# Optimization experiments

Hardware: AMD Instinct MI355X
Metric: run time of the kernel (lower is better)

The kernel has to match this reference:

```python
import jax, jax.numpy as jnp
import numpy as np

B, T, C = 4, 2048, 1024
H = 16
D = C // H  # head_dim = 64


def setup_inputs() -> dict:
    key = jax.random.key(0)
    ks = jax.random.split(key, 9)
    s = 1.0 / np.sqrt(C)
    return {
        "x": jax.random.normal(ks[0], (B, T, C), dtype=jnp.float32),
        "Wk": jax.random.uniform(ks[1], (C, C), jnp.float32, -s, s),
        "bk": jax.random.uniform(ks[2], (C,), jnp.float32, -s, s),
        "Wq": jax.random.uniform(ks[3], (C, C), jnp.float32, -s, s),
        "bq": jax.random.uniform(ks[4], (C,), jnp.float32, -s, s),
        "Wv": jax.random.uniform(ks[5], (C, C), jnp.float32, -s, s),
        "bv": jax.random.uniform(ks[6], (C,), jnp.float32, -s, s),
        "Wp": jax.random.uniform(ks[7], (C, C), jnp.float32, -s, s),
        "bp": jax.random.uniform(ks[8], (C,), jnp.float32, -s, s),
    }


def reference(x, Wk, bk, Wq, bq, Wv, bv, Wp, bp):
    # projections -> (B, H, T, D)
    def split_heads(y):
        return y.reshape(B, T, H, D).transpose(0, 2, 1, 3)

    k = split_heads(x @ Wk.T + bk)
    q = split_heads(x @ Wq.T + bq)
    v = split_heads(x @ Wv.T + bv)

    att = jnp.einsum("bhtd,bhsd->bhts", q, k) / np.sqrt(D).astype(np.float32)
    causal = jnp.tril(jnp.ones((T, T), dtype=bool))
    att = jnp.where(causal, att, -jnp.inf)
    att = jax.nn.softmax(att, axis=-1)

    y = jnp.einsum("bhts,bhsd->bhtd", att, v)  # (B,H,T,D)
    y = y.transpose(0, 2, 1, 3).reshape(B, T, C)
    return y @ Wp.T + bp
```

## Files before the change

kernel.cpp:

```cpp
#include <hip/hip_runtime.h>
#include <hip/hip_bf16.h>

typedef unsigned short u16;
typedef unsigned int u32;
typedef short short8 __attribute__((ext_vector_type(8)));
typedef short short4v __attribute__((ext_vector_type(4)));
typedef float f32x4 __attribute__((ext_vector_type(4)));

#define MFMA16(a, b, c) __builtin_amdgcn_mfma_f32_16x16x32_bf16((a), (b), (c), 0, 0, 0)

constexpr int kB = 4, kT = 2048, kC = 1024, kH = 16, kD = 64;
constexpr int kBT = kB * kT;
constexpr long kQKV = (long)kB * kH * kT * kD;
constexpr float kSC = 0.125f * 1.4426950408889634f;

__device__ inline u16 f2bf(float f) {
    __hip_bfloat16 h = __float2bfloat16(f);
    return *reinterpret_cast<u16*>(&h);
}
__device__ inline u32 pkbf_trunc(float lo, float hi) {
    return __builtin_amdgcn_perm(__builtin_bit_cast(u32, hi),
                                 __builtin_bit_cast(u32, lo), 0x07060302u);
}
__device__ inline u32 pkbf_rne(float lo, float hi) {
    return ((u32)f2bf(hi) << 16) | (u32)f2bf(lo);
}

__device__ inline void cp16(const u16* g, u16* l) {
    __builtin_amdgcn_global_load_lds(
        (const __attribute__((address_space(1))) unsigned int*)g,
        (__attribute__((address_space(3))) unsigned int*)l, 16, 0, 0);
}

__global__ __launch_bounds__(256) void cast_kernel(
    const float* __restrict__ x,  const float* __restrict__ Wk,
    const float* __restrict__ Wq, const float* __restrict__ Wv,
    const float* __restrict__ Wp,
    u16* __restrict__ xb, u16* __restrict__ wkb, u16* __restrict__ wqb,
    u16* __restrict__ wvb, u16* __restrict__ wpb)
{
    const long id = (long)blockIdx.x * 256 + threadIdx.x;
    const float* src;
    u16* dst;
    long off;
    if (id < 2097152) {
        src = x; dst = xb; off = id;
    } else {
        const long w = (id - 2097152) >> 18;
        off = (id - 2097152) & 262143;
        src = (w == 0) ? Wk : (w == 1) ? Wq : (w == 2) ? Wv : Wp;
        dst = (w == 0) ? wkb : (w == 1) ? wqb : (w == 2) ? wvb : wpb;
    }
    f32x4 v = *(const f32x4*)&src[off * 4];
    short4v s = {(short)f2bf(v[0]), (short)f2bf(v[1]),
                 (short)f2bf(v[2]), (short)f2bf(v[3])};
    *(short4v*)&dst[off * 4] = s;
}

__global__ __launch_bounds__(256) void qkv_gemm_bf16(
    const u16* __restrict__ xb,
    const u16* __restrict__ wkb, const u16* __restrict__ wqb,
    const u16* __restrict__ wvb,
    const float* __restrict__ bk, const float* __restrict__ bq,
    const float* __restrict__ bv,
    u16* __restrict__ kw, u16* __restrict__ qw, u16* __restrict__ vw)
{
    __shared__ u16 As[128 * 32];
    __shared__ u16 Bs[128 * 32];
    const int tid = threadIdx.x;
    const int lane = tid & 63;
    const int wid = tid >> 6;
    const int l15 = lane & 15;
    const int quad = lane >> 4;
    const int m0 = blockIdx.x * 128;
    const int n0 = blockIdx.y * 128;
    const int z = blockIdx.z;

    const u16* W = (z == 0) ? wkb : (z == 1) ? wqb : wvb;
    const float* bias = (z == 0) ? bk : (z == 1) ? bq : bv;

    f32x4 zero = {0.f, 0.f, 0.f, 0.f};
    f32x4 acc[4][4];
#pragma unroll
    for (int i = 0; i < 4; ++i)
#pragma unroll
        for (int j = 0; j < 4; ++j) acc[i][j] = zero;

    const int wm = (wid & 1) * 64;
    const int wn = (wid >> 1) * 64;

    const int sRow = tid >> 2;
    const int sCol = (tid & 3) * 8;
    const int ldsOff = sRow * 32 + sCol;

    for (int k0 = 0; k0 < kC; k0 += 32) {
        cp16(&xb[(long)(m0 + sRow) * kC + k0 + sCol],      &As[ldsOff]);
        cp16(&xb[(long)(m0 + 64 + sRow) * kC + k0 + sCol], &As[64 * 32 + ldsOff]);
        cp16(&W[(long)(n0 + sRow) * kC + k0 + sCol],       &Bs[ldsOff]);
        cp16(&W[(long)(n0 + 64 + sRow) * kC + k0 + sCol],  &Bs[64 * 32 + ldsOff]);
        __syncthreads();
        short8 af[4], bfr[4];
#pragma unroll
        for (int mt = 0; mt < 4; ++mt)
            af[mt] = *(const short8*)&As[(wm + mt * 16 + l15) * 32 + quad * 8];
#pragma unroll
        for (int nt = 0; nt < 4; ++nt)
            bfr[nt] = *(const short8*)&Bs[(wn + nt * 16 + l15) * 32 + quad * 8];
#pragma unroll
        for (int mt = 0; mt < 4; ++mt)
#pragma unroll
            for (int nt = 0; nt < 4; ++nt)
                acc[mt][nt] = MFMA16(af[mt], bfr[nt], acc[mt][nt]);
        __syncthreads();
    }

    const float scale = (z == 1) ? kSC : 1.0f;
#pragma unroll
    for (int nt = 0; nt < 4; ++nt) {
        const int n = n0 + wn + nt * 16 + l15;
        const float bias_f = bias[n];
        const int h = n >> 6, d = n & 63;
#pragma unroll
        for (int mt = 0; mt < 4; ++mt) {
#pragma unroll
            for (int r = 0; r < 4; ++r) {
                const int m = m0 + wm + mt * 16 + quad * 4 + r;
                const int b = m >> 11, t = m & 2047;
                const float v = (acc[mt][nt][r] + bias_f) * scale;
                const int bh = b * kH + h;
                if (z == 2) {
                    vw[((long)bh * kD + d) * kT + t] = f2bf(v);
                } else {
                    u16* dst = (z == 0) ? kw : qw;
                    dst[((long)bh * kT + t) * kD + d] = f2bf(v);
                }
            }
        }
    }
}

__global__ __launch_bounds__(256) void qkv_gemm_kernel(
    const float* __restrict__ x,
    const float* __restrict__ Wk, const float* __restrict__ bk,
    const float* __restrict__ Wq, const float* __restrict__ bq,
    const float* __restrict__ Wv, const float* __restrict__ bv,
    u16* __restrict__ kw, u16* __restrict__ qw, u16* __restrict__ vw)
{
    __shared__ u16 As[128 * 32];
    __shared__ u16 Bs[128 * 32];
    const int tid = threadIdx.x;
    const int lane = tid & 63;
    const int wid = tid >> 6;
    const int l15 = lane & 15;
    const int quad = lane >> 4;
    const int m0 = blockIdx.x * 128;
    const int n0 = blockIdx.y * 128;
    const int z = blockIdx.z;

    const float* W = (z == 0) ? Wk : (z == 1) ? Wq : Wv;
    const float* bias = (z == 0) ? bk : (z == 1) ? bq : bv;

    f32x4 zero = {0.f, 0.f, 0.f, 0.f};
    f32x4 acc[4][4];
#pragma unroll
    for (int i = 0; i < 4; ++i)
#pragma unroll
        for (int j = 0; j < 4; ++j) acc[i][j] = zero;

    const int wm = (wid & 1) * 64;
    const int wn = (wid >> 1) * 64;
    const int row4 = tid >> 3;
    const int col4 = (tid & 7) * 4;

    for (int k0 = 0; k0 < kC; k0 += 32) {
#pragma unroll
        for (int p = 0; p < 4; ++p) {
            const int r = p * 32 + row4;
            f32x4 xa = *(const f32x4*)&x[(long)(m0 + r) * kC + k0 + col4];
            f32x4 wa = *(const f32x4*)&W[(long)(n0 + r) * kC + k0 + col4];
            short4v xs = {(short)f2bf(xa[0]), (short)f2bf(xa[1]),
                          (short)f2bf(xa[2]), (short)f2bf(xa[3])};
            short4v wsv = {(short)f2bf(wa[0]), (short)f2bf(wa[1]),
                           (short)f2bf(wa[2]), (short)f2bf(wa[3])};
            *(short4v*)&As[r * 32 + col4] = xs;
            *(short4v*)&Bs[r * 32 + col4] = wsv;
        }
        __syncthreads();
        short8 af[4], bfr[4];
#pragma unroll
        for (int mt = 0; mt < 4; ++mt)
            af[mt] = *(const short8*)&As[(wm + mt * 16 + l15) * 32 + quad * 8];
#pragma unroll
        for (int nt = 0; nt < 4; ++nt)
            bfr[nt] = *(const short8*)&Bs[(wn + nt * 16 + l15) * 32 + quad * 8];
#pragma unroll
        for (int mt = 0; mt < 4; ++mt)
#pragma unroll
            for (int nt = 0; nt < 4; ++nt)
                acc[mt][nt] = MFMA16(af[mt], bfr[nt], acc[mt][nt]);
        __syncthreads();
    }

    const float scale = (z == 1) ? kSC : 1.0f;
#pragma unroll
    for (int nt = 0; nt < 4; ++nt) {
        const int n = n0 + wn + nt * 16 + l15;
        const float bias_f = bias[n];
        const int h = n >> 6, d = n & 63;
#pragma unroll
        for (int mt = 0; mt < 4; ++mt) {
#pragma unroll
            for (int r = 0; r < 4; ++r) {
                const int m = m0 + wm + mt * 16 + quad * 4 + r;
                const int b = m >> 11, t = m & 2047;
                const float v = (acc[mt][nt][r] + bias_f) * scale;
                const int bh = b * kH + h;
                if (z == 2) {
                    vw[((long)bh * kD + d) * kT + t] = f2bf(v);
                } else {
                    u16* dst = (z == 0) ? kw : qw;
                    dst[((long)bh * kT + t) * kD + d] = f2bf(v);
                }
            }
        }
    }
}

__global__ __launch_bounds__(256) void attn_kernel(
    const u16* qw, const u16* kw, const u16* vw, u16* ow)
{
    __shared__ u16 Ks[2][64 * 64];
    __shared__ u16 VT[2][64 * 64];
    __shared__ u16 Pb[64 * 64];

    const int tid = threadIdx.x;
    const int lane = tid & 63;
    const int wid = tid >> 6;
    const int l15 = lane & 15;
    const int quad = lane >> 4;
    const int id = blockIdx.x;
    const int bh = id & 63;
    const int pr = id >> 6;

    const float NEG = -1.0e30f;
    f32x4 zero = {0.f, 0.f, 0.f, 0.f};
    const short8 onesf = {(short)0x3F80, (short)0x3F80, (short)0x3F80, (short)0x3F80,
                          (short)0x3F80, (short)0x3F80, (short)0x3F80, (short)0x3F80};

    const int r0 = tid >> 3;
    const int cc = tid & 7;
    const int r1 = r0 + 32;
    const int sw0 = r0 * 64 + ((cc ^ (r0 & 7)) * 8);
    const int sw1 = r1 * 64 + ((cc ^ (r1 & 7)) * 8);
    const int c0e = cc * 8;

    const int rl7 = l15 & 7;

    const u16* kbase = kw + (long)bh * kT * kD;
    const u16* vbase = vw + (long)bh * kD * kT;

#pragma unroll
    for (int ph = 0; ph < 2; ++ph) {
        const int qt64 = ph ? (31 - pr) : pr;
        const int tw = qt64 * 64 + wid * 16;

        short8 qf0, qf1;
        {
            const u16* qp = qw + ((long)bh * kT + tw + l15) * kD;
            qf0 = *(const short8*)&qp[quad * 8];
            qf1 = *(const short8*)&qp[32 + quad * 8];
        }

        f32x4 oacc[4];
#pragma unroll
        for (int mo = 0; mo < 4; ++mo) oacc[mo] = zero;
        f32x4 lsum = zero;

        const int n_st = qt64 + 1;

        const u16* kp0 = kbase + (long)r0 * kD + c0e;
        const u16* kp1 = kbase + (long)r1 * kD + c0e;
        const u16* vp0 = vbase + (long)r0 * kT + c0e;
        const u16* vp1 = vbase + (long)r1 * kT + c0e;
        short8 ka = *(const short8*)kp0;
        short8 kb = *(const short8*)kp1;
        short8 va = *(const short8*)vp0;
        short8 vb = *(const short8*)vp1;
        kp0 += 64 * kD; kp1 += 64 * kD;
        vp0 += 64;      vp1 += 64;
        __syncthreads();
        *(short8*)&Ks[0][sw0] = ka;
        *(short8*)&Ks[0][sw1] = kb;
        *(short8*)&VT[0][sw0] = va;
        *(short8*)&VT[0][sw1] = vb;
        if (n_st > 1) {
            ka = *(const short8*)kp0;
            kb = *(const short8*)kp1;
            va = *(const short8*)vp0;
            vb = *(const short8*)vp1;
            kp0 += 64 * kD; kp1 += 64 * kD;
            vp0 += 64;      vp1 += 64;
        }

        for (int st = 0; st < n_st; ++st) {
            __syncthreads();
            const int cur = st & 1;
            if (st + 1 < n_st) {
                const int nxt = cur ^ 1;
                *(short8*)&Ks[nxt][sw0] = ka;
                *(short8*)&Ks[nxt][sw1] = kb;
                *(short8*)&VT[nxt][sw0] = va;
                *(short8*)&VT[nxt][sw1] = vb;
            }
            if (st + 2 < n_st) {
                ka = *(const short8*)kp0;
                kb = *(const short8*)kp1;
                va = *(const short8*)vp0;
                vb = *(const short8*)vp1;
                kp0 += 64 * kD; kp1 += 64 * kD;
                vp0 += 64;      vp1 += 64;
            }

            short8 kf[4][2];
#pragma unroll
            for (int ms = 0; ms < 4; ++ms) {
                const int row = ms * 16 + l15;
#pragma unroll
                for (int k2 = 0; k2 < 2; ++k2)
                    kf[ms][k2] = *(const short8*)
                        &Ks[cur][row * 64 + (((k2 * 4 + quad) ^ rl7) * 8)];
            }
            f32x4 sacc[4];
#pragma unroll
            for (int ms = 0; ms < 4; ++ms) {
                sacc[ms] = MFMA16(kf[ms][0], qf0, zero);
                sacc[ms] = MFMA16(kf[ms][1], qf1, sacc[ms]);
            }

            if (st == n_st - 1) {
                const int tl = wid * 16 + l15;
#pragma unroll
                for (int ms = 0; ms < 4; ++ms)
#pragma unroll
                    for (int r = 0; r < 4; ++r)
                        if (ms * 16 + quad * 4 + r > tl) sacc[ms][r] = NEG;
            }

            const int prow = wid * 16 + l15;
#pragma unroll
            for (int ms = 0; ms < 4; ++ms) {
                const float p0 = exp2f(sacc[ms][0]);
                const float p1 = exp2f(sacc[ms][1]);
                const float p2 = exp2f(sacc[ms][2]);
                const float p3 = exp2f(sacc[ms][3]);
                uint2 pk;
                pk.x = pkbf_trunc(p0, p1);
                pk.y = pkbf_trunc(p2, p3);
                const int chunk = (ms * 2 + (quad >> 1)) ^ rl7;
                *(uint2*)&Pb[prow * 64 + chunk * 8 + (quad & 1) * 4] = pk;
            }

            short8 pf0 = *(const short8*)&Pb[prow * 64 + ((quad ^ rl7) * 8)];
            short8 pf1 = *(const short8*)&Pb[prow * 64 + (((4 + quad) ^ rl7) * 8)];
            lsum = MFMA16(onesf, pf0, lsum);
            lsum = MFMA16(onesf, pf1, lsum);
#pragma unroll
            for (int mo = 0; mo < 4; ++mo) {
                const int row = mo * 16 + l15;
                short8 vf0 = *(const short8*)
                    &VT[cur][row * 64 + ((quad ^ rl7) * 8)];
                short8 vf1 = *(const short8*)
                    &VT[cur][row * 64 + (((4 + quad) ^ rl7) * 8)];
                oacc[mo] = MFMA16(vf0, pf0, oacc[mo]);
                oacc[mo] = MFMA16(vf1, pf1, oacc[mo]);
            }
        }

        const float inv = 1.0f / lsum[0];
        const int t = tw + l15;
        u16* op = ow + ((long)bh * kT + t) * kD;
#pragma unroll
        for (int mo = 0; mo < 4; ++mo) {
            uint2 ov;
            ov.x = pkbf_rne(oacc[mo][0] * inv, oacc[mo][1] * inv);
            ov.y = pkbf_rne(oacc[mo][2] * inv, oacc[mo][3] * inv);
            *(uint2*)&op[mo * 16 + quad * 4] = ov;
        }
    }
}

__global__ __launch_bounds__(256) void out_gemm_bf16(
    const u16* __restrict__ ob, const u16* __restrict__ wpb,
    const float* __restrict__ bp, float* __restrict__ out)
{
    __shared__ u16 As[128 * 32];
    __shared__ u16 Bs[128 * 32];
    const int tid = threadIdx.x;
    const int lane = tid & 63;
    const int wid = tid >> 6;
    const int l15 = lane & 15;
    const int quad = lane >> 4;
    const int m0 = blockIdx.x * 128;
    const int n0 = blockIdx.y * 128;

    f32x4 zero = {0.f, 0.f, 0.f, 0.f};
    f32x4 acc[4][4];
#pragma unroll
    for (int i = 0; i < 4; ++i)
#pragma unroll
        for (int j = 0; j < 4; ++j) acc[i][j] = zero;

    const int wm = (wid & 1) * 64;
    const int wn = (wid >> 1) * 64;

    const int sRow = tid >> 2;
    const int sCol = (tid & 3) * 8;
    const int ldsOff = sRow * 32 + sCol;

    for (int k0 = 0; k0 < kC; k0 += 32) {
        const int h = k0 >> 6;
        const int d = (k0 & 63) + sCol;
        {
            const int m = m0 + sRow, b = m >> 11, t = m & 2047;
            cp16(&ob[(((long)b * kH + h) * kT + t) * kD + d], &As[ldsOff]);
        }
        {
            const int m = m0 + 64 + sRow, b = m >> 11, t = m & 2047;
            cp16(&ob[(((long)b * kH + h) * kT + t) * kD + d], &As[64 * 32 + ldsOff]);
        }
        cp16(&wpb[(long)(n0 + sRow) * kC + k0 + sCol],      &Bs[ldsOff]);
        cp16(&wpb[(long)(n0 + 64 + sRow) * kC + k0 + sCol], &Bs[64 * 32 + ldsOff]);
        __syncthreads();
        short8 af[4], bfr[4];
#pragma unroll
        for (int mt = 0; mt < 4; ++mt)
            af[mt] = *(const short8*)&As[(wm + mt * 16 + l15) * 32 + quad * 8];
#pragma unroll
        for (int nt = 0; nt < 4; ++nt)
            bfr[nt] = *(const short8*)&Bs[(wn + nt * 16 + l15) * 32 + quad * 8];
#pragma unroll
        for (int mt = 0; mt < 4; ++mt)
#pragma unroll
            for (int nt = 0; nt < 4; ++nt)
                acc[mt][nt] = MFMA16(af[mt], bfr[nt], acc[mt][nt]);
        __syncthreads();
    }

#pragma unroll
    for (int nt = 0; nt < 4; ++nt) {
        const int n = n0 + wn + nt * 16 + l15;
        const float bias_f = bp[n];
#pragma unroll
        for (int mt = 0; mt < 4; ++mt) {
#pragma unroll
            for (int r = 0; r < 4; ++r) {
                const int m = m0 + wm + mt * 16 + quad * 4 + r;
                out[(long)m * kC + n] = acc[mt][nt][r] + bias_f;
            }
        }
    }
}

__global__ __launch_bounds__(256) void out_gemm_kernel(
    const u16* __restrict__ ow, const float* __restrict__ Wp,
    const float* __restrict__ bp, float* __restrict__ out)
{
    __shared__ u16 As[128 * 32];
    __shared__ u16 Bs[128 * 32];
    const int tid = threadIdx.x;
    const int lane = tid & 63;
    const int wid = tid >> 6;
    const int l15 = lane & 15;
    const int quad = lane >> 4;
    const int m0 = blockIdx.x * 128;
    const int n0 = blockIdx.y * 128;

    f32x4 zero = {0.f, 0.f, 0.f, 0.f};
    f32x4 acc[4][4];
#pragma unroll
    for (int i = 0; i < 4; ++i)
#pragma unroll
        for (int j = 0; j < 4; ++j) acc[i][j] = zero;

    const int wm = (wid & 1) * 64;
    const int wn = (wid >> 1) * 64;

    const int r0 = tid >> 2;
    const int kkA = (tid & 3) * 8;
    const int r1 = r0 + 64;
    const int row4 = tid >> 3;
    const int col4 = (tid & 7) * 4;

    for (int k0 = 0; k0 < kC; k0 += 32) {
        {
            const int m = m0 + r0, b = m >> 11, t = m & 2047;
            const int kk = k0 + kkA, h = kk >> 6, d = kk & 63;
            *(short8*)&As[r0 * 32 + kkA] =
                *(const short8*)&ow[(((long)b * kH + h) * kT + t) * kD + d];
        }
        {
            const int m = m0 + r1, b = m >> 11, t = m & 2047;
            const int kk = k0 + kkA, h = kk >> 6, d = kk & 63;
            *(short8*)&As[r1 * 32 + kkA] =
                *(const short8*)&ow[(((long)b * kH + h) * kT + t) * kD + d];
        }
#pragma unroll
        for (int p = 0; p < 4; ++p) {
            const int r = p * 32 + row4;
            f32x4 wa = *(const f32x4*)&Wp[(long)(n0 + r) * kC + k0 + col4];
            short4v wsv = {(short)f2bf(wa[0]), (short)f2bf(wa[1]),
                           (short)f2bf(wa[2]), (short)f2bf(wa[3])};
            *(short4v*)&Bs[r * 32 + col4] = wsv;
        }
        __syncthreads();
        short8 af[4], bfr[4];
#pragma unroll
        for (int mt = 0; mt < 4; ++mt)
            af[mt] = *(const short8*)&As[(wm + mt * 16 + l15) * 32 + quad * 8];
#pragma unroll
        for (int nt = 0; nt < 4; ++nt)
            bfr[nt] = *(const short8*)&Bs[(wn + nt * 16 + l15) * 32 + quad * 8];
#pragma unroll
        for (int mt = 0; mt < 4; ++mt)
#pragma unroll
            for (int nt = 0; nt < 4; ++nt)
                acc[mt][nt] = MFMA16(af[mt], bfr[nt], acc[mt][nt]);
        __syncthreads();
    }

#pragma unroll
    for (int nt = 0; nt < 4; ++nt) {
        const int n = n0 + wn + nt * 16 + l15;
        const float bias_f = bp[n];
#pragma unroll
        for (int mt = 0; mt < 4; ++mt) {
#pragma unroll
            for (int r = 0; r < 4; ++r) {
                const int m = m0 + wm + mt * 16 + quad * 4 + r;
                out[(long)m * kC + n] = acc[mt][nt][r] + bias_f;
            }
        }
    }
}

extern "C" void kernel_launch(void* const* d_in, const int* in_sizes, int n_in,
                              void* d_out, int out_size, void* d_ws, size_t ws_size,
                              hipStream_t stream) {
    const float* x  = (const float*)d_in[0];
    const float* Wk = (const float*)d_in[1];
    const float* bk = (const float*)d_in[2];
    const float* Wq = (const float*)d_in[3];
    const float* bq = (const float*)d_in[4];
    const float* Wv = (const float*)d_in[5];
    const float* bv = (const float*)d_in[6];
    const float* Wp = (const float*)d_in[7];
    const float* bp = (const float*)d_in[8];
    float* out = (float*)d_out;

    u16* ws = (u16*)d_ws;
    const size_t kNeed = 72ull * 1024 * 1024;

    if (ws_size >= kNeed) {
        u16* k_ws = ws;
        u16* q_ws = ws + kQKV;
        u16* v_ws = ws + 2 * kQKV;
        u16* xb   = ws + 3 * kQKV;
        u16* o_ws = xb;
        u16* wkb  = ws + 4 * kQKV;
        u16* wqb  = wkb + (long)kC * kC;
        u16* wvb  = wqb + (long)kC * kC;
        u16* wpb  = wvb + (long)kC * kC;

        cast_kernel<<<12288, 256, 0, stream>>>(x, Wk, Wq, Wv, Wp,
                                               xb, wkb, wqb, wvb, wpb);
        qkv_gemm_bf16<<<dim3(kBT / 128, kC / 128, 3), 256, 0, stream>>>(
            xb, wkb, wqb, wvb, bk, bq, bv, k_ws, q_ws, v_ws);
        attn_kernel<<<1024, 256, 0, stream>>>(q_ws, k_ws, v_ws, o_ws);
        out_gemm_bf16<<<dim3(kBT / 128, kC / 128), 256, 0, stream>>>(
            o_ws, wpb, bp, out);
    } else {
        u16* k_ws = ws;
        u16* q_ws = ws + kQKV;
        u16* v_ws = ws + 2 * kQKV;
        u16* o_ws = q_ws;

        qkv_gemm_kernel<<<dim3(kBT / 128, kC / 128, 3), 256, 0, stream>>>(
            x, Wk, bk, Wq, bq, Wv, bv, k_ws, q_ws, v_ws);
        attn_kernel<<<1024, 256, 0, stream>>>(q_ws, k_ws, v_ws, o_ws);
        out_gemm_kernel<<<dim3(kBT / 128, kC / 128), 256, 0, stream>>>(
            o_ws, Wp, bp, out);
    }
}
```

Baseline: 282.7 us.

## Halve attention block to two waves each handling 32 query rows with async K/V staging

The attention kernel now runs with 128 threads, and each wave processes two 16-row query groups. Each K and V fragment read from shared memory is therefore reused across two MFMA groups, which halves LDS fragment traffic per unit of work. K/V tile loads switch from register-staged global loads to a cp16 helper writing directly into the swizzled LDS buffers. s_setprio hints are placed around the MFMA sections. The trade-off is higher register pressure per wave and fewer waves per block to hide latency, and the change relies on a cp16 helper defined elsewhere.

```diff
diff --git a/kernel.cpp b/kernel.cpp
--- a/kernel.cpp
+++ b/kernel.cpp
@@ -226,7 +226,7 @@
     }
 }
 
-__global__ __launch_bounds__(256) void attn_kernel(
+__global__ __launch_bounds__(128, 2) void attn_kernel(
     const u16* qw, const u16* kw, const u16* vw, u16* ow)
 {
     __shared__ u16 Ks[2][64 * 64];
@@ -247,144 +247,146 @@
     const short8 onesf = {(short)0x3F80, (short)0x3F80, (short)0x3F80, (short)0x3F80,
                           (short)0x3F80, (short)0x3F80, (short)0x3F80, (short)0x3F80};
 
-    const int r0 = tid >> 3;
-    const int cc = tid & 7;
-    const int r1 = r0 + 32;
-    const int sw0 = r0 * 64 + ((cc ^ (r0 & 7)) * 8);
-    const int sw1 = r1 * 64 + ((cc ^ (r1 & 7)) * 8);
-    const int c0e = cc * 8;
-
     const int rl7 = l15 & 7;
 
     const u16* kbase = kw + (long)bh * kT * kD;
     const u16* vbase = vw + (long)bh * kD * kT;
 
+    const u16* kp[4];
+    const u16* vp[4];
+#pragma unroll
+    for (int q = 0; q < 4; ++q) {
+        const int slot = q * 128 + tid;
+        const int row = slot >> 3;
+        const int c = slot & 7;
+        const int off = (c ^ (row & 7)) * 8;
+        kp[q] = kbase + (long)row * kD + off;
+        vp[q] = vbase + (long)row * kT + off;
+    }
+
+    auto stage = [&](int buf, int st) {
+        u16* kd = Ks[buf];
+        u16* vd = VT[buf];
+#pragma unroll
+        for (int q = 0; q < 4; ++q) {
+            cp16(kp[q] + (long)st * (64 * kD), kd + (q * 128 + tid) * 8);
+            cp16(vp[q] + st * 64,              vd + (q * 128 + tid) * 8);
+        }
+    };
+
 #pragma unroll
     for (int ph = 0; ph < 2; ++ph) {
         const int qt64 = ph ? (31 - pr) : pr;
-        const int tw = qt64 * 64 + wid * 16;
-
-        short8 qf0, qf1;
-        {
-            const u16* qp = qw + ((long)bh * kT + tw + l15) * kD;
-            qf0 = *(const short8*)&qp[quad * 8];
-            qf1 = *(const short8*)&qp[32 + quad * 8];
-        }
-
-        f32x4 oacc[4];
-#pragma unroll
-        for (int mo = 0; mo < 4; ++mo) oacc[mo] = zero;
-        f32x4 lsum = zero;
-
+        const int tw = qt64 * 64 + wid * 32;
         const int n_st = qt64 + 1;
 
-        const u16* kp0 = kbase + (long)r0 * kD + c0e;
-        const u16* kp1 = kbase + (long)r1 * kD + c0e;
-        const u16* vp0 = vbase + (long)r0 * kT + c0e;
-        const u16* vp1 = vbase + (long)r1 * kT + c0e;
-        short8 ka = *(const short8*)kp0;
-        short8 kb = *(const short8*)kp1;
-        short8 va = *(const short8*)vp0;
-        short8 vb = *(const short8*)vp1;
-        kp0 += 64 * kD; kp1 += 64 * kD;
-        vp0 += 64;      vp1 += 64;
-        __syncthreads();
-        *(short8*)&Ks[0][sw0] = ka;
-        *(short8*)&Ks[0][sw1] = kb;
-        *(short8*)&VT[0][sw0] = va;
-        *(short8*)&VT[0][sw1] = vb;
-        if (n_st > 1) {
-            ka = *(const short8*)kp0;
-            kb = *(const short8*)kp1;
-            va = *(const short8*)vp0;
-            vb = *(const short8*)vp1;
-            kp0 += 64 * kD; kp1 += 64 * kD;
-            vp0 += 64;      vp1 += 64;
-        }
+        __syncthreads();
+        stage(0, 0);
+
+        short8 qf[2][2];
+#pragma unroll
+        for (int g = 0; g < 2; ++g) {
+            const u16* qp = qw + ((long)bh * kT + tw + g * 16 + l15) * kD;
+            qf[g][0] = *(const short8*)&qp[quad * 8];
+            qf[g][1] = *(const short8*)&qp[32 + quad * 8];
+        }
+
+        f32x4 oacc[4][2];
+#pragma unroll
+        for (int mo = 0; mo < 4; ++mo)
+#pragma unroll
+            for (int g = 0; g < 2; ++g) oacc[mo][g] = zero;
+        f32x4 lsum[2] = {zero, zero};
 
         for (int st = 0; st < n_st; ++st) {
             __syncthreads();
             const int cur = st & 1;
-            if (st + 1 < n_st) {
-                const int nxt = cur ^ 1;
-                *(short8*)&Ks[nxt][sw0] = ka;
-                *(short8*)&Ks[nxt][sw1] = kb;
-                *(short8*)&VT[nxt][sw0] = va;
-                *(short8*)&VT[nxt][sw1] = vb;
-            }
-            if (st + 2 < n_st) {
-                ka = *(const short8*)kp0;
-                kb = *(const short8*)kp1;
-                va = *(const short8*)vp0;
-                vb = *(const short8*)vp1;
-                kp0 += 64 * kD; kp1 += 64 * kD;
-                vp0 += 64;      vp1 += 64;
-            }
-
-            short8 kf[4][2];
+            if (st + 1 < n_st) stage(cur ^ 1, st + 1);
+
+            const u16* K_ = Ks[cur];
+            const u16* V_ = VT[cur];
+
+            f32x4 sacc[4][2];
+            __builtin_amdgcn_s_setprio(1);
 #pragma unroll
             for (int ms = 0; ms < 4; ++ms) {
                 const int row = ms * 16 + l15;
-#pragma unroll
-                for (int k2 = 0; k2 < 2; ++k2)
-                    kf[ms][k2] = *(const short8*)
-                        &Ks[cur][row * 64 + (((k2 * 4 + quad) ^ rl7) * 8)];
-            }
-            f32x4 sacc[4];
-#pragma unroll
-            for (int ms = 0; ms < 4; ++ms) {
-                sacc[ms] = MFMA16(kf[ms][0], qf0, zero);
-                sacc[ms] = MFMA16(kf[ms][1], qf1, sacc[ms]);
-            }
+                short8 kf0 = *(const short8*)&K_[row * 64 + ((quad ^ rl7) * 8)];
+                short8 kf1 = *(const short8*)&K_[row * 64 + (((4 + quad) ^ rl7) * 8)];
+#pragma unroll
+                for (int g = 0; g < 2; ++g) {
+                    sacc[ms][g] = MFMA16(kf0, qf[g][0], zero);
+                    sacc[ms][g] = MFMA16(kf1, qf[g][1], sacc[ms][g]);
+                }
+            }
+            __builtin_amdgcn_s_setprio(0);
 
             if (st == n_st - 1) {
-                const int tl = wid * 16 + l15;
-#pragma unroll
-                for (int ms = 0; ms < 4; ++ms)
-#pragma unroll
-                    for (int r = 0; r < 4; ++r)
-                        if (ms * 16 + quad * 4 + r > tl) sacc[ms][r] = NEG;
-            }
-
-            const int prow = wid * 16 + l15;
-#pragma unroll
-            for (int ms = 0; ms < 4; ++ms) {
-                const float p0 = exp2f(sacc[ms][0]);
-                const float p1 = exp2f(sacc[ms][1]);
-                const float p2 = exp2f(sacc[ms][2]);
-                const float p3 = exp2f(sacc[ms][3]);
-                uint2 pk;
-                pk.x = pkbf_trunc(p0, p1);
-                pk.y = pkbf_trunc(p2, p3);
-                const int chunk = (ms * 2 + (quad >> 1)) ^ rl7;
-                *(uint2*)&Pb[prow * 64 + chunk * 8 + (quad & 1) * 4] = pk;
-            }
-
-            short8 pf0 = *(const short8*)&Pb[prow * 64 + ((quad ^ rl7) * 8)];
-            short8 pf1 = *(const short8*)&Pb[prow * 64 + (((4 + quad) ^ rl7) * 8)];
-            lsum = MFMA16(onesf, pf0, lsum);
-            lsum = MFMA16(onesf, pf1, lsum);
+#pragma unroll
+                for (int g = 0; g < 2; ++g) {
+                    const int tl = wid * 32 + g * 16 + l15;
+#pragma unroll
+                    for (int ms = 0; ms < 4; ++ms)
+#pragma unroll
+                        for (int r = 0; r < 4; ++r)
+                            if (ms * 16 + quad * 4 + r > tl) sacc[ms][g][r] = NEG;
+                }
+            }
+
+#pragma unroll
+            for (int g = 0; g < 2; ++g) {
+                const int prow = wid * 32 + g * 16 + l15;
+#pragma unroll
+                for (int ms = 0; ms < 4; ++ms) {
+                    const float p0 = exp2f(sacc[ms][g][0]);
+                    const float p1 = exp2f(sacc[ms][g][1]);
+                    const float p2 = exp2f(sacc[ms][g][2]);
+                    const float p3 = exp2f(sacc[ms][g][3]);
+                    uint2 pk;
+                    pk.x = pkbf_trunc(p0, p1);
+                    pk.y = pkbf_trunc(p2, p3);
+                    const int chunk = (ms * 2 + (quad >> 1)) ^ rl7;
+                    *(uint2*)&Pb[prow * 64 + chunk * 8 + (quad & 1) * 4] = pk;
+                }
+            }
+
+            short8 pf[2][2];
+#pragma unroll
+            for (int g = 0; g < 2; ++g) {
+                const int prow = wid * 32 + g * 16 + l15;
+                pf[g][0] = *(const short8*)&Pb[prow * 64 + ((quad ^ rl7) * 8)];
+                pf[g][1] = *(const short8*)&Pb[prow * 64 + (((4 + quad) ^ rl7) * 8)];
+                lsum[g] = MFMA16(onesf, pf[g][0], lsum[g]);
+                lsum[g] = MFMA16(onesf, pf[g][1], lsum[g]);
+            }
+
+            __builtin_amdgcn_s_setprio(1);
 #pragma unroll
             for (int mo = 0; mo < 4; ++mo) {
                 const int row = mo * 16 + l15;
-                short8 vf0 = *(const short8*)
-                    &VT[cur][row * 64 + ((quad ^ rl7) * 8)];
-                short8 vf1 = *(const short8*)
-                    &VT[cur][row * 64 + (((4 + quad) ^ rl7) * 8)];
-                oacc[mo] = MFMA16(vf0, pf0, oacc[mo]);
-                oacc[mo] = MFMA16(vf1, pf1, oacc[mo]);
-            }
-        }
-
-        const float inv = 1.0f / lsum[0];
-        const int t = tw + l15;
-        u16* op = ow + ((long)bh * kT + t) * kD;
-#pragma unroll
-        for (int mo = 0; mo < 4; ++mo) {
-            uint2 ov;
-            ov.x = pkbf_rne(oacc[mo][0] * inv, oacc[mo][1] * inv);
-            ov.y = pkbf_rne(oacc[mo][2] * inv, oacc[mo][3] * inv);
-            *(uint2*)&op[mo * 16 + quad * 4] = ov;
+                short8 vf0 = *(const short8*)&V_[row * 64 + ((quad ^ rl7) * 8)];
+                short8 vf1 = *(const short8*)&V_[row * 64 + (((4 + quad) ^ rl7) * 8)];
+#pragma unroll
+                for (int g = 0; g < 2; ++g) {
+                    oacc[mo][g] = MFMA16(vf0, pf[g][0], oacc[mo][g]);
+                    oacc[mo][g] = MFMA16(vf1, pf[g][1], oacc[mo][g]);
+                }
+            }
+            __builtin_amdgcn_s_setprio(0);
+        }
+
+#pragma unroll
+        for (int g = 0; g < 2; ++g) {
+            const float inv = 1.0f / lsum[g][0];
+            const int t = tw + g * 16 + l15;
+            u16* op = ow + ((long)bh * kT + t) * kD;
+#pragma unroll
+            for (int mo = 0; mo < 4; ++mo) {
+                uint2 ov;
+                ov.x = pkbf_rne(oacc[mo][g][0] * inv, oacc[mo][g][1] * inv);
+                ov.y = pkbf_rne(oacc[mo][g][2] * inv, oacc[mo][g][3] * inv);
+                *(uint2*)&op[mo * 16 + quad * 4] = ov;
+            }
         }
     }
 }
@@ -575,7 +577,7 @@
                                                xb, wkb, wqb, wvb, wpb);
         qkv_gemm_bf16<<<dim3(kBT / 128, kC / 128, 3), 256, 0, stream>>>(
             xb, wkb, wqb, wvb, bk, bq, bv, k_ws, q_ws, v_ws);
-        attn_kernel<<<1024, 256, 0, stream>>>(q_ws, k_ws, v_ws, o_ws);
+        attn_kernel<<<1024, 128, 0, stream>>>(q_ws, k_ws, v_ws, o_ws);
         out_gemm_bf16<<<dim3(kBT / 128, kC / 128), 256, 0, stream>>>(
             o_ws, wpb, bp, out);
     } else {
@@ -586,7 +588,7 @@
 
         qkv_gemm_kernel<<<dim3(kBT / 128, kC / 128, 3), 256, 0, stream>>>(
             x, Wk, bk, Wq, bq, Wv, bv, k_ws, q_ws, v_ws);
-        attn_kernel<<<1024, 256, 0, stream>>>(q_ws, k_ws, v_ws, o_ws);
+        attn_kernel<<<1024, 128, 0, stream>>>(q_ws, k_ws, v_ws, o_ws);
         out_gemm_kernel<<<dim3(kBT / 128, kC / 128), 256, 0, stream>>>(
             o_ws, Wp, bp, out);
     }
```

Measured after the change: 266.9 us. 1.06x faster.
